# Performance work log

Measured on AMD Instinct MI355X. Metric: run time of the kernel, lower is better.

The kernel has to match this reference:

```python
import jax, jax.numpy as jnp
import numpy as np

B, C, H, W = 2, 48, 128, 256
HEADS = 3
EPS_LN = 1e-6
EPS_NRM = 1e-12


def _conv(x, w, b, padding=0, dilation=1, groups=1):
    # x: NCHW, w: OIHW
    out = jax.lax.conv_general_dilated(
        x, w, window_strides=(1, 1),
        padding=[(padding, padding), (padding, padding)],
        rhs_dilation=(dilation, dilation),
        feature_group_count=groups,
        dimension_numbers=('NCHW', 'OIHW', 'NCHW'))
    return out + b[None, :, None, None]


def _ln2d(x, w, b):
    # LayerNorm over channel dim per pixel (NAFNet-style LayerNorm2d)
    mu = x.mean(axis=1, keepdims=True)
    var = ((x - mu) ** 2).mean(axis=1, keepdims=True)
    return (x - mu) / jnp.sqrt(var + EPS_LN) * w[None, :, None, None] + b[None, :, None, None]


def _l2norm(x):
    # F.normalize(dim=-1): x / max(||x||_2, eps)
    n = jnp.sqrt((x * x).sum(-1, keepdims=True))
    return x / jnp.maximum(n, EPS_NRM)


def setup_inputs() -> dict:
    key = jax.random.key(0)
    ks = iter(jax.random.split(key, 40))
    def nrm(shape, s=0.02):
        return jax.random.normal(next(ks), shape, jnp.float32) * s
    d = {
        'x_l': jax.random.normal(next(ks), (B, C, H, W), jnp.float32),
        'x_r': jax.random.normal(next(ks), (B, C, H, W), jnp.float32),
        'ln1_w': jnp.ones((C,), jnp.float32), 'ln1_b': jnp.zeros((C,), jnp.float32),
        'ln2_w': jnp.ones((C,), jnp.float32), 'ln2_b': jnp.zeros((C,), jnp.float32),
        'qkv_l_w': nrm((3 * C, C, 1, 1)), 'qkv_l_b': jnp.zeros((3 * C,), jnp.float32),
        'qkv_r_w': nrm((3 * C, C, 1, 1)), 'qkv_r_b': jnp.zeros((3 * C,), jnp.float32),
        'dw_l_w': nrm((3 * C, 1, 3, 3)), 'dw_l_b': jnp.zeros((3 * C,), jnp.float32),
        'dw_r_w': nrm((3 * C, 1, 3, 3)), 'dw_r_b': jnp.zeros((3 * C,), jnp.float32),
        'dil0_w': nrm((2 * C, 2 * C, 3, 3)), 'dil0_b': jnp.zeros((2 * C,), jnp.float32),
        'dil1_w': nrm((2 * C, 2 * C, 3, 3)), 'dil1_b': jnp.zeros((2 * C,), jnp.float32),
        'dil2_w': nrm((2 * C, 2 * C, 3, 3)), 'dil2_b': jnp.zeros((2 * C,), jnp.float32),
        'convQ_w': nrm((C, 6 * C, 1, 1)), 'convQ_b': jnp.zeros((C,), jnp.float32),
        'conv1_w': nrm((C, C, 1, 1)), 'conv1_b': jnp.zeros((C,), jnp.float32),
        'conv2_w': nrm((C, C, 1, 1)), 'conv2_b': jnp.zeros((C,), jnp.float32),
        'temperature': jnp.ones((HEADS, 1, 1), jnp.float32),
    }
    return d


def reference(x_l, x_r, ln1_w, ln1_b, ln2_w, ln2_b,
              qkv_l_w, qkv_l_b, qkv_r_w, qkv_r_b,
              dw_l_w, dw_l_b, dw_r_w, dw_r_b,
              dil0_w, dil0_b, dil1_w, dil1_b, dil2_w, dil2_b,
              convQ_w, convQ_b, conv1_w, conv1_b, conv2_w, conv2_b,
              temperature):
    b, c, h, w = x_l.shape
    hw = h * w
    ch = c // HEADS  # channels per head

    norm_l = _ln2d(x_l, ln1_w, ln1_b)
    norm_r = _ln2d(x_r, ln2_w, ln2_b)

    qkvl = _conv(_conv(norm_l, qkv_l_w, qkv_l_b), dw_l_w, dw_l_b, padding=1, groups=3 * c)
    qkvr = _conv(_conv(norm_r, qkv_r_w, qkv_r_b), dw_r_w, dw_r_b, padding=1, groups=3 * c)
    Q_l, K_l, V_l = jnp.split(qkvl, 3, axis=1)
    Q_r, K_r, V_r = jnp.split(qkvr, 3, axis=1)

    Q = jnp.concatenate((Q_l, Q_r), axis=1)  # [b, 2c, h, w]
    Q = jnp.concatenate((
        _conv(Q, dil0_w, dil0_b, padding=2, dilation=2),
        _conv(Q, dil1_w, dil1_b, padding=4, dilation=4),
        _conv(Q, dil2_w, dil2_b, padding=6, dilation=6)), axis=1)  # [b, 6c, h, w]
    Q = _conv(Q, convQ_w, convQ_b)  # [b, c, h, w]

    def heads(t):
        return t.reshape(b, HEADS, ch, hw)

    Q = _l2norm(heads(Q))
    K_l = _l2norm(heads(K_l))
    K_r = _l2norm(heads(K_r))
    V_l = heads(V_l)
    V_r = heads(V_r)

    # channel attention: [b, head, ch, ch]
    A_r2l = jax.nn.softmax(jnp.einsum('bhcn,bhdn->bhcd', Q, K_r) * temperature, axis=-1)
    A_l2r = jax.nn.softmax(jnp.einsum('bhcn,bhdn->bhcd', Q, K_l) * temperature, axis=-1)

    F_l = jnp.einsum('bhcd,bhdn->bhcn', A_r2l, V_l).reshape(b, c, h, w)
    F_r = jnp.einsum('bhcd,bhdn->bhcn', A_l2r, V_r).reshape(b, c, h, w)

    F_l = _conv(F_l, conv1_w, conv1_b)
    F_r = _conv(F_r, conv2_w, conv2_b)
    return (x_l + F_l, x_r + F_r)
```

## Files before the change

kernel.cpp:

```cpp
#include <hip/hip_runtime.h>
#include <hip/hip_bf16.h>

typedef __hip_bfloat16 bf16;
typedef __attribute__((ext_vector_type(8))) short short8;
typedef __attribute__((ext_vector_type(4))) float f32x4;

constexpr int IMG_H = 128;
constexpr int IMG_W = 256;
constexpr int HW    = IMG_H * IMG_W;
constexpr int BB    = 2;
constexpr int CC    = 48;
constexpr int C3    = 144;
constexpr int XPW   = 268;
constexpr int XOFF  = 6;

constexpr int WO_QKVL_W = 0;
constexpr int WO_QKVR_W = 6912;
constexpr int WO_DWL_W  = 13824;
constexpr int WO_DWR_W  = 15120;
constexpr int WO_C1_W   = 16416;
constexpr int WO_C2_W   = 18720;
constexpr int WO_QKVL_B = 21024;
constexpr int WO_QKVR_B = 21168;
constexpr int WO_DWL_B  = 21312;
constexpr int WO_DWR_B  = 21456;
constexpr int WO_C1_B   = 21600;
constexpr int WO_C2_B   = 21648;
constexpr int WO_LN1W   = 21696;
constexpr int WO_LN1B   = 21744;
constexpr int WO_LN2W   = 21792;
constexpr int WO_LN2B   = 21840;
constexpr int WO_TEMP   = 21888;
constexpr int WO_WQ     = 21952;
constexpr int WO_D0W    = 35776;
constexpr int WO_D1W    = 118720;
constexpr int WO_D2W    = 201664;
constexpr int WO_BQ     = 284608;
constexpr int WO_B0     = 284656;
constexpr int WO_B1     = 284752;
constexpr int WO_B2     = 284848;
constexpr int WO_WPACK  = 284944;
constexpr int WO_EFFB   = 409360;
constexpr int WO_NQ     = 409424;
constexpr int WO_NKL    = 409520;
constexpr int WO_NKR    = 409616;
constexpr int WO_AR2L   = 409712;
constexpr int WO_AL2R   = 411248;
constexpr int WO_M1     = 412800;
constexpr int WO_M2     = 417408;
constexpr int WO_WQP    = 422016;

constexpr size_t ACT_BASE_BYTES = 1725440;

constexpr size_t A_P  = 0;
constexpr size_t A_Q1 = 9437184;
constexpr size_t A_Q2 = 18874368;
constexpr size_t A_QC = 28311552;

struct PrepArgs {
  const void* src[25];
  int dst[25];
  int n[25];
};

__device__ __forceinline__ bool probe_bf16(const void* ln1w) {
  return ((const unsigned short*)ln1w)[0] == 0x3F80;
}

__global__ __launch_bounds__(256) void prep_k(PrepArgs a, float* __restrict__ wsf) {
  bool isb = probe_bf16(a.src[12]);
  int t = blockIdx.y;
  int i = blockIdx.x * 256 + threadIdx.x;
  if (i < a.n[t]) {
    float v = isb ? __bfloat162float(((const bf16*)a.src[t])[i])
                  : ((const float*)a.src[t])[i];
    wsf[a.dst[t] + i] = v;
  }
}

__global__ __launch_bounds__(256) void effw2_k(const float* __restrict__ wsf,
                                               bf16* __restrict__ wpack) {
  int d  = blockIdx.x / 96;
  int ci = blockIdx.x % 96;
  __shared__ float wds[864];
  __shared__ float wqs[48 * 97];
  const int wdb = (d == 0) ? WO_D0W : (d == 1) ? WO_D1W : WO_D2W;
  for (int idx = threadIdx.x; idx < 864; idx += 256) {
    int m = idx / 9, tt = idx % 9;
    wds[idx] = wsf[wdb + (m * 96 + ci) * 9 + tt];
  }
  for (int idx = threadIdx.x; idx < 4608; idx += 256) {
    int co = idx / 96, m = idx % 96;
    wqs[co * 97 + m] = wsf[WO_WQ + co * 288 + d * 96 + m];
  }
  __syncthreads();
  int tco = threadIdx.x;
  if (tco < 432) {
    int t = tco / 48, co = tco % 48;
    float s = 0.f;
#pragma unroll 8
    for (int m = 0; m < 96; ++m) s += wqs[co * 97 + m] * wds[m * 9 + t];
    int kc = ci >> 5, j = ci & 7;
    int L = ((ci & 31) >> 3) * 16 + (co & 15);
    int nt = co >> 4;
    int f = ((d * 9 + t) * 3 + kc) * 3 + nt;
    wpack[(size_t)f * 512 + L * 8 + j] = __float2bfloat16(s);
  }
}

__global__ __launch_bounds__(64) void effb_k(const float* __restrict__ wsf,
                                             float* __restrict__ effb) {
  int co = threadIdx.x;
  if (co >= 48) return;
  float s = wsf[WO_BQ + co];
  for (int m = 0; m < 96; ++m) {
    s += wsf[WO_WQ + co * 288 + m]       * wsf[WO_B0 + m];
    s += wsf[WO_WQ + co * 288 + 96 + m]  * wsf[WO_B1 + m];
    s += wsf[WO_WQ + co * 288 + 192 + m] * wsf[WO_B2 + m];
  }
  effb[co] = s;
}

__global__ __launch_bounds__(256) void wqp_k(const float* __restrict__ wsf,
                                             bf16* __restrict__ wqp) {
  int idx = blockIdx.x * 256 + threadIdx.x;
  if (idx >= 18432) return;
  int side = idx / 9216;
  int rem = idx % 9216;
  int nt = rem / 1024;
  int kt = (rem / 512) % 2;
  int e  = rem % 512;
  int L = e >> 3, j = e & 7;
  int o = nt * 16 + (L & 15);
  int kp = kt * 32 + (L >> 4) * 8 + j;
  int g = kp >> 4, r = kp & 15;
  float val = 0.f;
  if (r < 12) {
    int c = g * 12 + r;
    val = wsf[(side ? WO_QKVR_W : WO_QKVL_W) + o * 48 + c];
  }
  wqp[idx] = __float2bfloat16(val);
}

__global__ __launch_bounds__(256) void ln_k(
    const void* __restrict__ x, const void* __restrict__ probe,
    const float* __restrict__ lnw, const float* __restrict__ lnb,
    bf16* __restrict__ xn) {
  int px = threadIdx.x & 63;
  int w  = threadIdx.x >> 6;
  int p  = blockIdx.x * 64 + px;
  int b  = p >> 15;
  int pix = p & (HW - 1);
  size_t base = (size_t)b * CC * HW + pix;
  float v[12];
  if (probe_bf16(probe)) {
    const bf16* xp = (const bf16*)x + base;
#pragma unroll
    for (int c = 0; c < 12; ++c)
      v[c] = __bfloat162float(xp[(size_t)(w * 12 + c) * HW]);
  } else {
    const float* xp = (const float*)x + base;
#pragma unroll
    for (int c = 0; c < 12; ++c) v[c] = xp[(size_t)(w * 12 + c) * HW];
  }
  float s = 0.f, s2 = 0.f;
#pragma unroll
  for (int c = 0; c < 12; ++c) { s += v[c]; s2 += v[c] * v[c]; }
  __shared__ float2 red[4][64];
  red[w][px] = make_float2(s, s2);
  __syncthreads();
  float S = 0.f, S2 = 0.f;
#pragma unroll
  for (int i = 0; i < 4; ++i) { S += red[i][px].x; S2 += red[i][px].y; }
  float mu = S * (1.f / 48.f);
  float var = S2 * (1.f / 48.f) - mu * mu;
  float rs = rsqrtf(var + 1e-6f);
  bf16 o[16];
#pragma unroll
  for (int c = 0; c < 12; ++c)
    o[c] = __float2bfloat16((v[c] - mu) * rs * lnw[w * 12 + c] + lnb[w * 12 + c]);
#pragma unroll
  for (int c = 12; c < 16; ++c) o[c] = __float2bfloat16(0.f);
  bf16* dst = xn + (size_t)p * 64 + w * 16;
  *(uint4*)(dst) = *(uint4*)(o);
  *(uint4*)(dst + 8) = *(uint4*)(o + 8);
}

__global__ __launch_bounds__(256) void qkv_mfma_k(
    const bf16* __restrict__ xn, const bf16* __restrict__ wqp_side,
    const float* __restrict__ qb, bf16* __restrict__ pre) {
  __shared__ __align__(16) bf16 W[18 * 512];
  __shared__ __align__(16) bf16 Cs[144][72];
  for (int i = threadIdx.x; i < 1152; i += 256)
    ((uint4*)W)[i] = ((const uint4*)wqp_side)[i];
  __syncthreads();
  int L = threadIdx.x & 63, w = threadIdx.x >> 6;
  int lo = L & 15, hi = L >> 4;
  int p0 = blockIdx.x * 64 + w * 16;
  const bf16* abase = xn + (size_t)(p0 + lo) * 64 + hi * 8;
  short8 a0 = *(const short8*)(abase);
  short8 a1 = *(const short8*)(abase + 32);
#pragma unroll
  for (int nt = 0; nt < 9; ++nt) {
    float bv = qb[nt * 16 + lo];
    f32x4 acc = {bv, bv, bv, bv};
    acc = __builtin_amdgcn_mfma_f32_16x16x32_bf16(
        a0, *(const short8*)(W + (nt * 2 + 0) * 512 + L * 8), acc, 0, 0, 0);
    acc = __builtin_amdgcn_mfma_f32_16x16x32_bf16(
        a1, *(const short8*)(W + (nt * 2 + 1) * 512 + L * 8), acc, 0, 0, 0);
#pragma unroll
    for (int r = 0; r < 4; ++r)
      Cs[nt * 16 + lo][w * 16 + hi * 4 + r] = __float2bfloat16(acc[r]);
  }
  __syncthreads();
  int b = (blockIdx.x * 64) >> 15;
  int pix0 = (blockIdx.x * 64) & (HW - 1);
#pragma unroll
  for (int pass = 0; pass < 18; ++pass) {
    int o = pass * 8 + (threadIdx.x >> 5);
    int px = (threadIdx.x & 31) * 2;
    bf16 t2[2];
    t2[0] = Cs[o][px];
    t2[1] = Cs[o][px + 1];
    *(unsigned*)(pre + ((size_t)(b * C3 + o)) * HW + pix0 + px) = *(unsigned*)t2;
  }
}

__global__ __launch_bounds__(256) void dw_k(
    const bf16* __restrict__ in, const float* __restrict__ w9,
    const float* __restrict__ bias, bf16* __restrict__ out) {
  int gid = blockIdx.x;
  int yt = gid & 15;
  int c = (gid >> 4) % C3;
  int b = gid / (16 * C3);
  int ry = threadIdx.x >> 5, xi = threadIdx.x & 31;
  int y = yt * 8 + ry;
  int x0 = xi * 8;
  const bf16* base = in + ((size_t)(b * C3 + c)) * HW;
  float wv[9];
#pragma unroll
  for (int t = 0; t < 9; ++t) wv[t] = w9[c * 9 + t];
  float bz = bias[c];
  float acc[8];
#pragma unroll
  for (int i = 0; i < 8; ++i) acc[i] = bz;
#pragma unroll
  for (int ky = 0; ky < 3; ++ky) {
    int yy = y + ky - 1;
    if ((unsigned)yy >= (unsigned)IMG_H) continue;
    const bf16* row = base + yy * IMG_W + x0;
    uint4 m = *(const uint4*)(row);
    float f[10];
    f[0] = (x0 > 0) ? __bfloat162float(row[-1]) : 0.f;
    f[9] = (x0 + 8 < IMG_W) ? __bfloat162float(row[8]) : 0.f;
    f[1] = __uint_as_float(m.x << 16);
    f[2] = __uint_as_float(m.x & 0xFFFF0000u);
    f[3] = __uint_as_float(m.y << 16);
    f[4] = __uint_as_float(m.y & 0xFFFF0000u);
    f[5] = __uint_as_float(m.z << 16);
    f[6] = __uint_as_float(m.z & 0xFFFF0000u);
    f[7] = __uint_as_float(m.w << 16);
    f[8] = __uint_as_float(m.w & 0xFFFF0000u);
    float w0 = wv[ky * 3], w1 = wv[ky * 3 + 1], w2 = wv[ky * 3 + 2];
#pragma unroll
    for (int i = 0; i < 8; ++i)
      acc[i] += w0 * f[i] + w1 * f[i + 1] + w2 * f[i + 2];
  }
  bf16 o[8];
#pragma unroll
  for (int i = 0; i < 8; ++i) o[i] = __float2bfloat16(acc[i]);
  *(uint4*)(out + ((size_t)(b * C3 + c)) * HW + y * IMG_W + x0) = *(uint4*)o;
}

__global__ __launch_bounds__(256) void qc_k(const bf16* __restrict__ q1,
                                            const bf16* __restrict__ q2,
                                            bf16* __restrict__ qc) {
  int b = blockIdx.x >> 7;
  int y = blockIdx.x & 127;
  int half = blockIdx.y;
  int tid = threadIdx.x;
  int x0 = half * 128;
  int px = tid & 127;
  int cig = tid >> 7;
  __shared__ __align__(16) bf16 T[128][100];
#pragma unroll 8
  for (int k = 0; k < 48; ++k) {
    int ci = cig * 48 + k;
    const bf16* src = (ci < 48)
        ? q1 + (((size_t)(b * C3 + ci)) * IMG_H + y) * IMG_W
        : q2 + (((size_t)(b * C3 + ci - 48)) * IMG_H + y) * IMG_W;
    T[px][ci] = src[x0 + px];
  }
  __syncthreads();
  size_t rowbase = ((size_t)(b * IMG_H + y)) * XPW * 96 + (size_t)half * 12864;
#pragma unroll 1
  for (int i = 0; i < 13; ++i) {
    int e4 = i * 256 + tid;
    if (e4 >= 3216) break;
    int e = e4 * 4;
    int xp = (e + half * 12864) / 96;
    int ci = (e + half * 12864) % 96;
    int x = xp - XOFF;
    uint2 val;
    if ((unsigned)x < (unsigned)IMG_W) {
      val = *(const uint2*)(&T[x - x0][ci]);
    } else {
      val.x = 0u; val.y = 0u;
    }
    *(uint2*)(qc + rowbase + e) = val;
  }
}

__global__ __launch_bounds__(256) void dil_mfma_k(
    const bf16* __restrict__ qc, const bf16* __restrict__ wp,
    const float* __restrict__ effb, bf16* __restrict__ qh) {
  int tid = threadIdx.x;
  int L = tid & 63;
  int w = tid >> 6;
  int lo = L & 15, hi = L >> 4;
  int x0 = blockIdx.x * 64;
  int y = blockIdx.y;
  int b = blockIdx.z;
  int px = x0 + w * 16 + lo;

  f32x4 acc[3];
#pragma unroll
  for (int nt = 0; nt < 3; ++nt) {
    float bv = effb[nt * 16 + lo];
    acc[nt][0] = bv; acc[nt][1] = bv; acc[nt][2] = bv; acc[nt][3] = bv;
  }

  const size_t arow0 = ((size_t)(b * IMG_H + y) * XPW + XOFF + px) * 96 + hi * 8;

#pragma unroll
  for (int d = 0; d < 3; ++d) {
    const int D = 2 * (d + 1);
#pragma unroll
    for (int t = 0; t < 9; ++t) {
      const int dy = (t / 3 - 1) * D;
      const int dx = (t % 3 - 1) * D;
      int yy = y + dy;
      if ((unsigned)yy >= (unsigned)IMG_H) continue;
      const bf16* arow = qc + arow0 + ((long)dy * XPW + dx) * 96;
      const bf16* wrow = wp + (size_t)((d * 9 + t) * 9) * 512 + L * 8;
#pragma unroll
      for (int kc = 0; kc < 3; ++kc) {
        short8 a = *(const short8*)(arow + kc * 32);
        const bf16* wb = wrow + (size_t)kc * 3 * 512;
        acc[0] = __builtin_amdgcn_mfma_f32_16x16x32_bf16(
            a, *(const short8*)(wb), acc[0], 0, 0, 0);
        acc[1] = __builtin_amdgcn_mfma_f32_16x16x32_bf16(
            a, *(const short8*)(wb + 512), acc[1], 0, 0, 0);
        acc[2] = __builtin_amdgcn_mfma_f32_16x16x32_bf16(
            a, *(const short8*)(wb + 1024), acc[2], 0, 0, 0);
      }
    }
  }

  __shared__ __align__(16) float Cs[48][68];
#pragma unroll
  for (int nt = 0; nt < 3; ++nt)
#pragma unroll
    for (int r = 0; r < 4; ++r)
      Cs[nt * 16 + lo][w * 16 + hi * 4 + r] = acc[nt][r];
  __syncthreads();
#pragma unroll
  for (int i = 0; i < 3; ++i) {
    int e4 = (i * 256 + tid);
    int co = e4 >> 4;
    int px4 = (e4 & 15) * 4;
    const float* src = &Cs[co][px4];
    bf16 tmp[4];
    tmp[0] = __float2bfloat16(src[0]);
    tmp[1] = __float2bfloat16(src[1]);
    tmp[2] = __float2bfloat16(src[2]);
    tmp[3] = __float2bfloat16(src[3]);
    *(uint2*)(qh + (((size_t)(b * CC + co)) * IMG_H + y) * IMG_W + x0 + px4) =
        *(uint2*)tmp;
  }
}

__device__ __forceinline__ float wave_sum(float v) {
#pragma unroll
  for (int off = 32; off > 0; off >>= 1) v += __shfl_down(v, off, 64);
  return v;
}

__device__ __forceinline__ float blo(unsigned u) {
  return __uint_as_float(u << 16);
}
__device__ __forceinline__ float bhi(unsigned u) {
  return __uint_as_float(u & 0xFFFF0000u);
}

__global__ __launch_bounds__(256) void rownorm_k(
    const bf16* __restrict__ qh, const bf16* __restrict__ qkvl,
    const bf16* __restrict__ qkvr, float* __restrict__ nq,
    float* __restrict__ nkl, float* __restrict__ nkr) {
  int id = blockIdx.x;
  int which = id / 96;
  int rid = id % 96;
  int b = rid / 48;
  int c = rid % 48;
  const bf16* ptr = (which == 0) ? qh + ((size_t)(b * CC + c)) * HW
                  : (which == 1) ? qkvl + ((size_t)(b * C3 + 48 + c)) * HW
                                 : qkvr + ((size_t)(b * C3 + 48 + c)) * HW;
  float s = 0.f;
#pragma unroll 2
  for (int it = 0; it < 16; ++it) {
    int n0 = (it * 256 + threadIdx.x) * 8;
    uint4 u = *(const uint4*)(ptr + n0);
    float a0 = blo(u.x), a1 = bhi(u.x), a2 = blo(u.y), a3 = bhi(u.y);
    float a4 = blo(u.z), a5 = bhi(u.z), a6 = blo(u.w), a7 = bhi(u.w);
    s += a0 * a0 + a1 * a1 + a2 * a2 + a3 * a3 + a4 * a4 + a5 * a5 +
         a6 * a6 + a7 * a7;
  }
  s = wave_sum(s);
  __shared__ float red[4];
  if ((threadIdx.x & 63) == 0) red[threadIdx.x >> 6] = s;
  __syncthreads();
  if (threadIdx.x == 0) {
    float tot = red[0] + red[1] + red[2] + red[3];
    float* dst = (which == 0) ? nq : (which == 1) ? nkl : nkr;
    dst[rid] = tot;
  }
}

__global__ __launch_bounds__(256) void logits_k(
    const bf16* __restrict__ qh, const bf16* __restrict__ qkvl,
    const bf16* __restrict__ qkvr, const float* __restrict__ nq,
    const float* __restrict__ nkl, const float* __restrict__ nkr,
    const float* __restrict__ temp, float* __restrict__ logr2l,
    float* __restrict__ logl2r) {
  int id = blockIdx.x;
  int a = id / 1536;
  int rem = id % 1536;
  int b = rem / 768;
  int h = (rem / 256) % 3;
  int i = (rem / 16) % 16;
  int j = rem % 16;
  const bf16* qrow = qh + ((size_t)(b * CC + h * 16 + i)) * HW;
  const bf16* krow = ((a == 0) ? qkvr : qkvl) + ((size_t)(b * C3 + 48 + h * 16 + j)) * HW;
  float s = 0.f;
#pragma unroll 2
  for (int it = 0; it < 16; ++it) {
    int n0 = (it * 256 + threadIdx.x) * 8;
    uint4 qu = *(const uint4*)(qrow + n0);
    uint4 ku = *(const uint4*)(krow + n0);
    s += blo(qu.x) * blo(ku.x) + bhi(qu.x) * bhi(ku.x);
    s += blo(qu.y) * blo(ku.y) + bhi(qu.y) * bhi(ku.y);
    s += blo(qu.z) * blo(ku.z) + bhi(qu.z) * bhi(ku.z);
    s += blo(qu.w) * blo(ku.w) + bhi(qu.w) * bhi(ku.w);
  }
  s = wave_sum(s);
  __shared__ float red[4];
  if ((threadIdx.x & 63) == 0) red[threadIdx.x >> 6] = s;
  __syncthreads();
  if (threadIdx.x == 0) {
    float tot = red[0] + red[1] + red[2] + red[3];
    float qn = fmaxf(sqrtf(nq[b * 48 + h * 16 + i]), 1e-12f);
    float kn = fmaxf(sqrtf(((a == 0) ? nkr : nkl)[b * 48 + h * 16 + j]), 1e-12f);
    float val = tot / (qn * kn) * temp[h];
    ((a == 0) ? logr2l : logl2r)[rem] = val;
  }
}

__global__ __launch_bounds__(256) void softmaxM_k(float* __restrict__ wsf) {
  int tid = threadIdx.x;
  __shared__ float A1[1536], A2[1536];
  if (tid < 192) {
    const float* p = wsf + ((tid < 96) ? WO_AR2L : WO_AL2R) + (tid % 96) * 16;
    float* dst = ((tid < 96) ? A1 : A2) + (tid % 96) * 16;
    float m = -1e30f;
#pragma unroll
    for (int j = 0; j < 16; ++j) m = fmaxf(m, p[j]);
    float s = 0.f;
    float e[16];
#pragma unroll
    for (int j = 0; j < 16; ++j) {
      e[j] = expf(p[j] - m);
      s += e[j];
    }
    float inv = 1.f / s;
#pragma unroll
    for (int j = 0; j < 16; ++j) dst[j] = e[j] * inv;
  }
  __syncthreads();
#pragma unroll 1
  for (int idx = tid; idx < 4608; idx += 256) {
    int b = idx / 2304;
    int r = idx % 2304;
    int o = r / 48;
    int cp = r % 48;
    int h = cp >> 4, j = cp & 15;
    const float* a1 = &A1[((b * 3 + h) * 16) * 16 + j];
    const float* a2 = &A2[((b * 3 + h) * 16) * 16 + j];
    float s1 = 0.f, s2 = 0.f;
#pragma unroll
    for (int i = 0; i < 16; ++i) {
      s1 += wsf[WO_C1_W + o * 48 + h * 16 + i] * a1[i * 16];
      s2 += wsf[WO_C2_W + o * 48 + h * 16 + i] * a2[i * 16];
    }
    wsf[WO_M1 + idx] = s1;
    wsf[WO_M2 + idx] = s2;
  }
}

__global__ __launch_bounds__(256) void attn_out2_k(
    const bf16* __restrict__ qkv, const void* __restrict__ x,
    const void* __restrict__ probe, const float* __restrict__ M,
    const float* __restrict__ cb, void* __restrict__ out, int half) {
  int tid = threadIdx.x;
  int p = blockIdx.x * 256 + tid;
  int b = __builtin_amdgcn_readfirstlane(p >> 15);
  int pix = p & (HW - 1);
  int o0 = blockIdx.y * 16;
  bool isb = probe_bf16(probe);

  float v[CC];
  const bf16* vb = qkv + ((size_t)(b * C3 + 96)) * HW + pix;
#pragma unroll
  for (int c = 0; c < CC; ++c) v[c] = __bfloat162float(vb[(size_t)c * HW]);

  const float* Mb = M + b * 2304;
  size_t base = (size_t)b * CC * HW + pix;
  float res[16];
#pragma unroll 2
  for (int o = 0; o < 16; ++o) {
    float acc = cb[o0 + o];
    const float* mrow = Mb + (o0 + o) * 48;
#pragma unroll
    for (int c = 0; c < CC; ++c) acc += mrow[c] * v[c];
    res[o] = acc;
  }
  size_t obase = (size_t)half * BB * CC * HW + base + (size_t)o0 * HW;
  if (isb) {
    const bf16* xp = (const bf16*)x + base + (size_t)o0 * HW;
    bf16* op = (bf16*)out + obase;
#pragma unroll
    for (int o = 0; o < 16; ++o)
      op[(size_t)o * HW] =
          __float2bfloat16(res[o] + __bfloat162float(xp[(size_t)o * HW]));
  } else {
    const float* xp = (const float*)x + base + (size_t)o0 * HW;
    float* op = (float*)out + obase;
#pragma unroll
    for (int o = 0; o < 16; ++o) op[(size_t)o * HW] = res[o] + xp[(size_t)o * HW];
  }
}

extern "C" void kernel_launch(void* const* d_in, const int* in_sizes, int n_in,
                              void* d_out, int out_size, void* d_ws, size_t ws_size,
                              hipStream_t stream) {
  (void)in_sizes; (void)n_in; (void)out_size; (void)ws_size;
  const void* x_l = d_in[0];
  const void* x_r = d_in[1];
  const void* probe = d_in[2];
  float* wsf = (float*)d_ws;
  bf16* wpack = (bf16*)(wsf + WO_WPACK);
  bf16* wqp = (bf16*)(wsf + WO_WQP);
  bf16* act = (bf16*)((char*)d_ws + ACT_BASE_BYTES);
  bf16* P  = act + A_P;
  bf16* Q1 = act + A_Q1;
  bf16* Q2 = act + A_Q2;
  bf16* QC = act + A_QC;
  bf16* XN = act + A_QC;
  bf16* qh = P;

  PrepArgs pa;
  const int srcIdx[25] = {6, 8, 10, 12, 22, 24, 7, 9, 11, 13, 23, 25,
                          2, 3, 4, 5, 26, 20, 14, 16, 18, 21, 15, 17, 19};
  const int dstOff[25] = {WO_QKVL_W, WO_QKVR_W, WO_DWL_W, WO_DWR_W, WO_C1_W, WO_C2_W,
                          WO_QKVL_B, WO_QKVR_B, WO_DWL_B, WO_DWR_B, WO_C1_B, WO_C2_B,
                          WO_LN1W, WO_LN1B, WO_LN2W, WO_LN2B, WO_TEMP,
                          WO_WQ, WO_D0W, WO_D1W, WO_D2W, WO_BQ, WO_B0, WO_B1, WO_B2};
  const int ns[25] = {6912, 6912, 1296, 1296, 2304, 2304, 144, 144, 144, 144,
                      48, 48, 48, 48, 48, 48, 3,
                      13824, 82944, 82944, 82944, 48, 96, 96, 96};
  for (int i = 0; i < 25; ++i) {
    pa.src[i] = d_in[srcIdx[i]];
    pa.dst[i] = dstOff[i];
    pa.n[i] = ns[i];
  }
  prep_k<<<dim3(324, 25), 256, 0, stream>>>(pa, wsf);

  effw2_k<<<288, 256, 0, stream>>>(wsf, wpack);
  effb_k<<<1, 64, 0, stream>>>(wsf, wsf + WO_EFFB);
  wqp_k<<<72, 256, 0, stream>>>(wsf, wqp);

  ln_k<<<1024, 256, 0, stream>>>(x_l, probe, wsf + WO_LN1W, wsf + WO_LN1B, XN);
  qkv_mfma_k<<<1024, 256, 0, stream>>>(XN, wqp, wsf + WO_QKVL_B, P);
  dw_k<<<BB * C3 * 16, 256, 0, stream>>>(P, wsf + WO_DWL_W, wsf + WO_DWL_B, Q1);
  ln_k<<<1024, 256, 0, stream>>>(x_r, probe, wsf + WO_LN2W, wsf + WO_LN2B, XN);
  qkv_mfma_k<<<1024, 256, 0, stream>>>(XN, wqp + 9216, wsf + WO_QKVR_B, P);
  dw_k<<<BB * C3 * 16, 256, 0, stream>>>(P, wsf + WO_DWR_W, wsf + WO_DWR_B, Q2);

  qc_k<<<dim3(BB * IMG_H, 2), 256, 0, stream>>>(Q1, Q2, QC);

  dil_mfma_k<<<dim3(IMG_W / 64, IMG_H, BB), 256, 0, stream>>>(
      QC, wpack, wsf + WO_EFFB, qh);

  rownorm_k<<<288, 256, 0, stream>>>(qh, Q1, Q2, wsf + WO_NQ,
                                     wsf + WO_NKL, wsf + WO_NKR);
  logits_k<<<3072, 256, 0, stream>>>(qh, Q1, Q2, wsf + WO_NQ,
                                     wsf + WO_NKL, wsf + WO_NKR,
                                     wsf + WO_TEMP, wsf + WO_AR2L, wsf + WO_AL2R);
  softmaxM_k<<<1, 256, 0, stream>>>(wsf);

  attn_out2_k<<<dim3(256, 3), 256, 0, stream>>>(
      Q1, x_l, probe, wsf + WO_M1, wsf + WO_C1_B, d_out, 0);
  attn_out2_k<<<dim3(256, 3), 256, 0, stream>>>(
      Q2, x_r, probe, wsf + WO_M2, wsf + WO_C2_B, d_out, 1);
}
```

Baseline: 313.3 us.

## Stage dilated-conv weights in LDS with wider tiles; compute logits via MFMA partials

The dilated conv kernel now processes 128 pixels per block (two 16-pixel subtiles per wave) and double-buffers each tap's weight slice in shared memory, so every weight fragment is reused across two MFMA streams instead of being re-read from global memory per wave. The channel-attention logits, previously one block per (i,j) pair doing scalar dot products over all pixels, are now computed with bf16 MFMA over pixel chunks, writing partial sums that a small reduction kernel combines and normalises. This trades per-tap barriers, more LDS and an extra partial-sum buffer and launch for far less redundant global traffic and scalar FMA work.

```diff
diff --git a/kernel.cpp b/kernel.cpp
--- a/kernel.cpp
+++ b/kernel.cpp
@@ -49,8 +49,9 @@
 constexpr int WO_M1     = 412800;
 constexpr int WO_M2     = 417408;
 constexpr int WO_WQP    = 422016;
-
-constexpr size_t ACT_BASE_BYTES = 1725440;
+constexpr int WO_PART   = 431232;
+
+constexpr size_t ACT_BASE_BYTES = 2118144;
 
 constexpr size_t A_P  = 0;
 constexpr size_t A_Q1 = 9437184;
@@ -314,69 +315,92 @@
 __global__ __launch_bounds__(256) void dil_mfma_k(
     const bf16* __restrict__ qc, const bf16* __restrict__ wp,
     const float* __restrict__ effb, bf16* __restrict__ qh) {
+  __shared__ __align__(16) unsigned char LDSU[26304];
+  bf16* Wb = (bf16*)LDSU;
+  float* Cs = (float*)LDSU;
   int tid = threadIdx.x;
   int L = tid & 63;
   int w = tid >> 6;
   int lo = L & 15, hi = L >> 4;
-  int x0 = blockIdx.x * 64;
+  int x0 = blockIdx.x * 128;
   int y = blockIdx.y;
   int b = blockIdx.z;
-  int px = x0 + w * 16 + lo;
-
-  f32x4 acc[3];
-#pragma unroll
-  for (int nt = 0; nt < 3; ++nt) {
-    float bv = effb[nt * 16 + lo];
-    acc[nt][0] = bv; acc[nt][1] = bv; acc[nt][2] = bv; acc[nt][3] = bv;
-  }
-
-  const size_t arow0 = ((size_t)(b * IMG_H + y) * XPW + XOFF + px) * 96 + hi * 8;
-
-#pragma unroll
-  for (int d = 0; d < 3; ++d) {
-    const int D = 2 * (d + 1);
-#pragma unroll
-    for (int t = 0; t < 9; ++t) {
-      const int dy = (t / 3 - 1) * D;
-      const int dx = (t % 3 - 1) * D;
-      int yy = y + dy;
-      if ((unsigned)yy >= (unsigned)IMG_H) continue;
-      const bf16* arow = qc + arow0 + ((long)dy * XPW + dx) * 96;
-      const bf16* wrow = wp + (size_t)((d * 9 + t) * 9) * 512 + L * 8;
+
+  f32x4 acc[2][3];
+#pragma unroll
+  for (int s = 0; s < 2; ++s)
+#pragma unroll
+    for (int nt = 0; nt < 3; ++nt) {
+      float bv = effb[nt * 16 + lo];
+      acc[s][nt] = {bv, bv, bv, bv};
+    }
+
+  const size_t abase =
+      ((size_t)(b * IMG_H + y) * XPW + XOFF + x0 + w * 32 + lo) * 96 + hi * 8;
+
+  {
+    const uint4* src = (const uint4*)(wp);
+    uint4* dst = (uint4*)(Wb);
+    dst[tid] = src[tid];
+    dst[tid + 256] = src[tid + 256];
+    if (tid < 64) dst[tid + 512] = src[tid + 512];
+  }
+  __syncthreads();
+
+#pragma unroll 1
+  for (int ti = 0; ti < 27; ++ti) {
+    if (ti + 1 < 27) {
+      const uint4* src = (const uint4*)(wp + (ti + 1) * 4608);
+      uint4* dst = (uint4*)(Wb + ((ti + 1) & 1) * 4608);
+      dst[tid] = src[tid];
+      dst[tid + 256] = src[tid + 256];
+      if (tid < 64) dst[tid + 512] = src[tid + 512];
+    }
+    int d = ti / 9, t = ti - d * 9;
+    int D = 2 * (d + 1);
+    int dy = (t / 3 - 1) * D;
+    int dx = (t % 3 - 1) * D;
+    int yy = y + dy;
+    if ((unsigned)yy < (unsigned)IMG_H) {
+      const bf16* wb = Wb + (ti & 1) * 4608 + L * 8;
+      const bf16* ap = qc + abase + ((long)dy * XPW + dx) * 96;
 #pragma unroll
       for (int kc = 0; kc < 3; ++kc) {
-        short8 a = *(const short8*)(arow + kc * 32);
-        const bf16* wb = wrow + (size_t)kc * 3 * 512;
-        acc[0] = __builtin_amdgcn_mfma_f32_16x16x32_bf16(
-            a, *(const short8*)(wb), acc[0], 0, 0, 0);
-        acc[1] = __builtin_amdgcn_mfma_f32_16x16x32_bf16(
-            a, *(const short8*)(wb + 512), acc[1], 0, 0, 0);
-        acc[2] = __builtin_amdgcn_mfma_f32_16x16x32_bf16(
-            a, *(const short8*)(wb + 1024), acc[2], 0, 0, 0);
+        short8 a0 = *(const short8*)(ap + kc * 32);
+        short8 a1 = *(const short8*)(ap + kc * 32 + 1536);
+        const bf16* wk = wb + kc * 3 * 512;
+#pragma unroll
+        for (int nt = 0; nt < 3; ++nt) {
+          short8 wv = *(const short8*)(wk + nt * 512);
+          acc[0][nt] = __builtin_amdgcn_mfma_f32_16x16x32_bf16(
+              a0, wv, acc[0][nt], 0, 0, 0);
+          acc[1][nt] = __builtin_amdgcn_mfma_f32_16x16x32_bf16(
+              a1, wv, acc[1][nt], 0, 0, 0);
+        }
       }
     }
-  }
-
-  __shared__ __align__(16) float Cs[48][68];
-#pragma unroll
-  for (int nt = 0; nt < 3; ++nt)
-#pragma unroll
-    for (int r = 0; r < 4; ++r)
-      Cs[nt * 16 + lo][w * 16 + hi * 4 + r] = acc[nt][r];
-  __syncthreads();
-#pragma unroll
-  for (int i = 0; i < 3; ++i) {
-    int e4 = (i * 256 + tid);
-    int co = e4 >> 4;
-    int px4 = (e4 & 15) * 4;
-    const float* src = &Cs[co][px4];
-    bf16 tmp[4];
-    tmp[0] = __float2bfloat16(src[0]);
-    tmp[1] = __float2bfloat16(src[1]);
-    tmp[2] = __float2bfloat16(src[2]);
-    tmp[3] = __float2bfloat16(src[3]);
-    *(uint2*)(qh + (((size_t)(b * CC + co)) * IMG_H + y) * IMG_W + x0 + px4) =
-        *(uint2*)tmp;
+    __syncthreads();
+  }
+
+#pragma unroll
+  for (int s = 0; s < 2; ++s)
+#pragma unroll
+    for (int nt = 0; nt < 3; ++nt)
+#pragma unroll
+      for (int r = 0; r < 4; ++r)
+        Cs[(nt * 16 + lo) * 137 + w * 32 + s * 16 + hi * 4 + r] = acc[s][nt][r];
+  __syncthreads();
+#pragma unroll
+  for (int it = 0; it < 3; ++it) {
+    int e = (it * 256 + tid) * 8;
+    int co = e >> 7;
+    int px = e & 127;
+    const float* srcp = &Cs[co * 137 + px];
+    bf16 tmp[8];
+#pragma unroll
+    for (int i2 = 0; i2 < 8; ++i2) tmp[i2] = __float2bfloat16(srcp[i2]);
+    *(uint4*)(qh + (((size_t)(b * CC + co)) * IMG_H + y) * IMG_W + x0 + px) =
+        *(uint4*)tmp;
   }
 }
 
@@ -426,43 +450,53 @@
   }
 }
 
-__global__ __launch_bounds__(256) void logits_k(
+__global__ __launch_bounds__(256) void logits_mfma_k(
     const bf16* __restrict__ qh, const bf16* __restrict__ qkvl,
-    const bf16* __restrict__ qkvr, const float* __restrict__ nq,
+    const bf16* __restrict__ qkvr, float* __restrict__ part) {
+  int abh = blockIdx.x;
+  int chunk = blockIdx.y;
+  int a = abh / 6;
+  int b = (abh / 3) % 2;
+  int h = abh % 3;
+  int tid = threadIdx.x;
+  int L = tid & 63, w = tid >> 6;
+  int lo = L & 15, hi = L >> 4;
+  const bf16* qrow = qh + ((size_t)(b * CC + h * 16 + lo)) * HW;
+  const bf16* krow =
+      ((a == 0) ? qkvr : qkvl) + ((size_t)(b * C3 + 48 + h * 16 + lo)) * HW;
+  int px0 = chunk * 1024 + w * 256 + hi * 8;
+  f32x4 acc = {0.f, 0.f, 0.f, 0.f};
+#pragma unroll
+  for (int s = 0; s < 8; ++s) {
+    short8 av = *(const short8*)(qrow + px0 + s * 32);
+    short8 bv = *(const short8*)(krow + px0 + s * 32);
+    acc = __builtin_amdgcn_mfma_f32_16x16x32_bf16(av, bv, acc, 0, 0, 0);
+  }
+  __shared__ float red[4][256];
+#pragma unroll
+  for (int r = 0; r < 4; ++r) red[w][(hi * 4 + r) * 16 + lo] = acc[r];
+  __syncthreads();
+  float sum = red[0][tid] + red[1][tid] + red[2][tid] + red[3][tid];
+  part[((size_t)abh * 32 + chunk) * 256 + tid] = sum;
+}
+
+__global__ __launch_bounds__(256) void logits_red_k(
+    const float* __restrict__ part, const float* __restrict__ nq,
     const float* __restrict__ nkl, const float* __restrict__ nkr,
     const float* __restrict__ temp, float* __restrict__ logr2l,
     float* __restrict__ logl2r) {
-  int id = blockIdx.x;
-  int a = id / 1536;
-  int rem = id % 1536;
-  int b = rem / 768;
-  int h = (rem / 256) % 3;
-  int i = (rem / 16) % 16;
-  int j = rem % 16;
-  const bf16* qrow = qh + ((size_t)(b * CC + h * 16 + i)) * HW;
-  const bf16* krow = ((a == 0) ? qkvr : qkvl) + ((size_t)(b * C3 + 48 + h * 16 + j)) * HW;
+  int abh = blockIdx.x;
+  int a = abh / 6, b = (abh / 3) % 2, h = abh % 3;
+  int t = threadIdx.x;
+  int i = t >> 4, j = t & 15;
   float s = 0.f;
-#pragma unroll 2
-  for (int it = 0; it < 16; ++it) {
-    int n0 = (it * 256 + threadIdx.x) * 8;
-    uint4 qu = *(const uint4*)(qrow + n0);
-    uint4 ku = *(const uint4*)(krow + n0);
-    s += blo(qu.x) * blo(ku.x) + bhi(qu.x) * bhi(ku.x);
-    s += blo(qu.y) * blo(ku.y) + bhi(qu.y) * bhi(ku.y);
-    s += blo(qu.z) * blo(ku.z) + bhi(qu.z) * bhi(ku.z);
-    s += blo(qu.w) * blo(ku.w) + bhi(qu.w) * bhi(ku.w);
-  }
-  s = wave_sum(s);
-  __shared__ float red[4];
-  if ((threadIdx.x & 63) == 0) red[threadIdx.x >> 6] = s;
-  __syncthreads();
-  if (threadIdx.x == 0) {
-    float tot = red[0] + red[1] + red[2] + red[3];
-    float qn = fmaxf(sqrtf(nq[b * 48 + h * 16 + i]), 1e-12f);
-    float kn = fmaxf(sqrtf(((a == 0) ? nkr : nkl)[b * 48 + h * 16 + j]), 1e-12f);
-    float val = tot / (qn * kn) * temp[h];
-    ((a == 0) ? logr2l : logl2r)[rem] = val;
-  }
+  const float* p = part + (size_t)abh * 32 * 256 + t;
+#pragma unroll 8
+  for (int c = 0; c < 32; ++c) s += p[c * 256];
+  float qn = fmaxf(sqrtf(nq[b * 48 + h * 16 + i]), 1e-12f);
+  float kn = fmaxf(sqrtf(((a == 0) ? nkr : nkl)[b * 48 + h * 16 + j]), 1e-12f);
+  float val = s / (qn * kn) * temp[h];
+  ((a == 0) ? logr2l : logl2r)[b * 768 + h * 256 + i * 16 + j] = val;
 }
 
 __global__ __launch_bounds__(256) void softmaxM_k(float* __restrict__ wsf) {
@@ -597,14 +631,16 @@
 
   qc_k<<<dim3(BB * IMG_H, 2), 256, 0, stream>>>(Q1, Q2, QC);
 
-  dil_mfma_k<<<dim3(IMG_W / 64, IMG_H, BB), 256, 0, stream>>>(
+  dil_mfma_k<<<dim3(IMG_W / 128, IMG_H, BB), 256, 0, stream>>>(
       QC, wpack, wsf + WO_EFFB, qh);
 
   rownorm_k<<<288, 256, 0, stream>>>(qh, Q1, Q2, wsf + WO_NQ,
                                      wsf + WO_NKL, wsf + WO_NKR);
-  logits_k<<<3072, 256, 0, stream>>>(qh, Q1, Q2, wsf + WO_NQ,
-                                     wsf + WO_NKL, wsf + WO_NKR,
-                                     wsf + WO_TEMP, wsf + WO_AR2L, wsf + WO_AL2R);
+  logits_mfma_k<<<dim3(12, 32), 256, 0, stream>>>(qh, Q1, Q2, wsf + WO_PART);
+  logits_red_k<<<12, 256, 0, stream>>>(wsf + WO_PART, wsf + WO_NQ,
+                                       wsf + WO_NKL, wsf + WO_NKR,
+                                       wsf + WO_TEMP, wsf + WO_AR2L,
+                                       wsf + WO_AL2R);
   softmaxM_k<<<1, 256, 0, stream>>>(wsf);
 
   attn_out2_k<<<dim3(256, 3), 256, 0, stream>>>(
```

Result: faster. 294.0 us (-6.2%).
